# Kernel optimization log

Hardware: AMD Instinct MI355X
Metric: run time of the kernel (lower is better)

The kernel has to match this reference:

```python
import jax, jax.numpy as jnp
from jax import lax
import numpy as np

# GatedLinearAttention: S_t = alpha_t * S_{t-1} + k_t^T v_t ; o_t = q_t @ S_t
DIM = 1024
H = 8
DK = 128   # dim*expand_k(1.0)/H
DV = 256   # dim*expand_v(2.0)/H
GATE_NORM = 16.0

def setup_inputs() -> dict:
    key = jax.random.key(0)
    ks = jax.random.split(key, 8)
    B, S = 2, 4096
    def xavier(k, shape, gain=1.0):
        fan_in, fan_out = shape[0], shape[1]
        lim = gain * np.sqrt(6.0 / (fan_in + fan_out))
        return jax.random.uniform(k, shape, jnp.float32, -lim, lim)
    g = 2 ** (-2.5)
    # weights stored as [in, out] so y = x @ W (transpose of torch Linear storage)
    return {
        "x":   jax.random.normal(ks[0], (B, S, DIM), jnp.float32),
        "Wq":  xavier(ks[1], (DIM, H * DK), g),
        "Wk":  xavier(ks[2], (DIM, H * DK), g),
        "Wv":  xavier(ks[3], (DIM, H * DV), g),
        "Wo":  xavier(ks[4], (H * DV, DIM)),
        "Wg":  xavier(ks[5], (DIM, H)),
        "bg":  jnp.zeros((H,), jnp.float32),
        "Wog": xavier(ks[6], (DIM, H * DV)),
    }

def _gla(x, Wq, Wk, Wv, Wo, Wg, bg, Wog):
    B, S, D = x.shape
    q = (x @ Wq).reshape(B, S, H, DK)
    k = (x @ Wk).reshape(B, S, H, DK) * (DK ** -0.5)
    v = (x @ Wv).reshape(B, S, H, DV)
    alpha = jax.nn.sigmoid((x @ Wg + bg) / GATE_NORM)  # [B,S,H]

    def step(state, inp):
        qt, kt, vt, at = inp  # [B,H,dk], [B,H,dk], [B,H,dv], [B,H]
        state = at[..., None, None] * state + kt[..., None] * vt[:, :, None, :]
        out_t = jnp.einsum('bhk,bhkv->bhv', qt, state)
        return state, out_t

    state0 = jnp.zeros((B, H, DK, DV), x.dtype)
    xs = (jnp.moveaxis(q, 1, 0), jnp.moveaxis(k, 1, 0),
          jnp.moveaxis(v, 1, 0), jnp.moveaxis(alpha, 1, 0))
    _, outs = lax.scan(step, state0, xs)          # [S,B,H,dv]
    out = jnp.moveaxis(outs, 0, 1).reshape(B, S, H * DV)
    og = jax.nn.sigmoid(x @ Wog)
    return (out * og) @ Wo

def reference(x, Wq, Wk, Wv, Wo, Wg, bg, Wog):
    return _gla(x, Wq, Wk, Wv, Wo, Wg, bg, Wog)
```

## Files before the change

### kernel.cpp

```cpp
#include <hip/hip_runtime.h>
#include <cstdint>
#include <cstddef>

typedef unsigned short u16;
typedef unsigned int   u32;
typedef __attribute__((ext_vector_type(8))) short short8;
typedef __attribute__((ext_vector_type(4))) float f32x4;

__device__ __forceinline__ u16 f2bf(float f) {
    union { float f; u32 u; } v; v.f = f;
    u32 r = v.u + 0x7fffu + ((v.u >> 16) & 1u);
    return (u16)(r >> 16);
}
__device__ __forceinline__ float bf2f(u16 b) {
    union { u32 u; float f; } v; v.u = ((u32)b) << 16;
    return v.f;
}

__device__ __forceinline__ void gload16(const u16* g, u16* l) {
    __builtin_amdgcn_global_load_lds(
        (const __attribute__((address_space(1))) u32*)g,
        (__attribute__((address_space(3))) u32*)l,
        16, 0, 0);
}

#define SEQ   4096
#define BATCH 2
#define NH    8
#define DKH   128
#define DVH   256
#define DMODEL 1024
#define NPROJ 6144
#define CHUNK 64
#define NCHUNK (SEQ / CHUNK)

#define OFF_XB    0u
#define OFF_WCAT  16777216u
#define OFF_WOT   29360128u
#define OFF_PROJ  33554432u
#define OFF_L2A   134217728u
#define OFF_GC    134479872u
#define OFF_U     134483968u
#define OFF_Z     201592832u

__global__ __launch_bounds__(256) void cvt_x_kernel(const float* __restrict__ x,
                                                    u16* __restrict__ xb) {
    int i = (blockIdx.x * 256 + threadIdx.x) * 4;
    float4 v = *(const float4*)(x + i);
    u16 o[4] = { f2bf(v.x), f2bf(v.y), f2bf(v.z), f2bf(v.w) };
    *(uint2*)(xb + i) = *(const uint2*)o;
}

__global__ __launch_bounds__(256) void transpose_w(const float* __restrict__ W, int N, int K,
                                                   u16* __restrict__ outp, float scale) {
    __shared__ float t[32][33];
    int n0 = blockIdx.x * 32, k0 = blockIdx.y * 32;
    int tx = threadIdx.x, ty = threadIdx.y;
    #pragma unroll
    for (int j = 0; j < 4; ++j)
        t[ty + j * 8][tx] = W[(size_t)(k0 + ty + j * 8) * N + n0 + tx];
    __syncthreads();
    #pragma unroll
    for (int j = 0; j < 4; ++j)
        outp[(size_t)(n0 + ty + j * 8) * K + k0 + tx] = f2bf(t[tx][ty + j * 8] * scale);
}

__global__ __launch_bounds__(256) void alpha_kernel(const float* __restrict__ x,
                                                    const float* __restrict__ Wg,
                                                    const float* __restrict__ bg,
                                                    float* __restrict__ l2a) {
    __shared__ float xr[DMODEL];
    int row = blockIdx.x;
    for (int i = threadIdx.x; i < DMODEL; i += 256) xr[i] = x[(size_t)row * DMODEL + i];
    __syncthreads();
    int wave = threadIdx.x >> 6, lane = threadIdx.x & 63;
    #pragma unroll
    for (int hh = 0; hh < 2; ++hh) {
        int h = wave * 2 + hh;
        float p = 0.f;
        for (int i = lane; i < DMODEL; i += 64) p += xr[i] * Wg[i * NH + h];
        #pragma unroll
        for (int d = 32; d; d >>= 1) p += __shfl_down(p, d, 64);
        if (lane == 0) {
            float zz = (p + bg[h]) * (1.0f / 16.0f);
            float a = 1.0f / (1.0f + expf(-zz));
            l2a[row * NH + h] = log2f(a);
        }
    }
}

template <int EPI>
__global__ __launch_bounds__(512, 2) void gemm256(const u16* __restrict__ A, int lda,
                                                  const u16* __restrict__ B, int ldb,
                                                  void* __restrict__ Cout, int ldc,
                                                  int K, int nTN, int og_start) {
    __shared__ u16 lds[65536];
    const int tid = threadIdx.x;
    const int lane = tid & 63, wid = tid >> 6;
    const int wr = wid >> 2, wc = wid & 3;
    const int cpx = gridDim.x >> 3;
    const int wg = (blockIdx.x & 7) * cpx + (blockIdx.x >> 3);
    const int m0 = (wg / nTN) * 256, n0 = (wg % nTN) * 256;

    const int rsub = tid >> 2;
    const int ql = (tid & 3) ^ ((tid >> 4) & 3);
    const size_t ag0 = (size_t)(m0 + rsub) * lda + ql * 8;
    const size_t ag1 = (size_t)(m0 + 128 + rsub) * lda + ql * 8;
    const size_t bg0 = (size_t)(n0 + rsub) * ldb + ql * 8;
    const size_t bg1 = (size_t)(n0 + 128 + rsub) * ldb + ql * 8;
    const int sdw = wid * 512;

#define STG_A(t_, h_) gload16(A + ((h_) ? ag1 : ag0) + (size_t)(t_) * 32, \
                              lds + ((t_) & 3) * 8192 + (h_) * 4096 + sdw)
#define STG_B(t_, h_) gload16(B + ((h_) ? bg1 : bg0) + (size_t)(t_) * 32, \
                              lds + 32768 + ((t_) & 3) * 8192 + (h_) * 4096 + sdw)

    const int qr = ((lane >> 4) ^ ((lane >> 2) & 3)) * 8;
    const int arow = (wr * 128 + (lane & 15)) * 32 + qr;
    const int brow = 32768 + (wc * 64 + (lane & 15)) * 32 + qr;

    STG_A(0, 0); STG_A(0, 1); STG_B(0, 0); STG_B(0, 1);
    STG_A(1, 0); STG_A(1, 1); STG_B(1, 0); STG_B(1, 1);
    asm volatile("s_waitcnt vmcnt(4)\n\ts_barrier" ::: "memory");

    f32x4 acc[8][4] = {};
    const int NT = K >> 5;
    for (int t = 0; t < NT; ++t) {
        const u16* buf = lds + (t & 3) * 8192;
        const bool pre = (t + 2) < NT;
        if (pre) { STG_A(t + 2, 0); STG_A(t + 2, 1); }
        short8 bfr[4], afr[4];
        #pragma unroll
        for (int ct = 0; ct < 4; ++ct) bfr[ct] = *(const short8*)(buf + brow + ct * 512);
        #pragma unroll
        for (int rt = 0; rt < 4; ++rt) afr[rt] = *(const short8*)(buf + arow + rt * 512);
        __builtin_amdgcn_s_setprio(1);
        #pragma unroll
        for (int rt = 0; rt < 4; ++rt)
            #pragma unroll
            for (int ct = 0; ct < 4; ++ct)
                acc[rt][ct] = __builtin_amdgcn_mfma_f32_16x16x32_bf16(afr[rt], bfr[ct], acc[rt][ct], 0, 0, 0);
        __builtin_amdgcn_s_setprio(0);
        if (pre) { STG_B(t + 2, 0); STG_B(t + 2, 1); }
        #pragma unroll
        for (int rt = 0; rt < 4; ++rt) afr[rt] = *(const short8*)(buf + arow + (rt + 4) * 512);
        __builtin_amdgcn_s_setprio(1);
        #pragma unroll
        for (int rt = 0; rt < 4; ++rt)
            #pragma unroll
            for (int ct = 0; ct < 4; ++ct)
                acc[rt + 4][ct] = __builtin_amdgcn_mfma_f32_16x16x32_bf16(afr[rt], bfr[ct], acc[rt + 4][ct], 0, 0, 0);
        __builtin_amdgcn_s_setprio(0);
        if (t < NT - 2)       asm volatile("s_waitcnt vmcnt(4)\n\ts_barrier" ::: "memory");
        else if (t == NT - 2) asm volatile("s_waitcnt vmcnt(0)\n\ts_barrier" ::: "memory");
    }
#undef STG_A
#undef STG_B

    __syncthreads();
    if (EPI) {
        u16* Cw = lds + wid * 4608;
        #pragma unroll
        for (int pass = 0; pass < 2; ++pass) {
            #pragma unroll
            for (int rt = 0; rt < 4; ++rt)
                #pragma unroll
                for (int ct = 0; ct < 4; ++ct)
                    #pragma unroll
                    for (int j = 0; j < 4; ++j) {
                        int row = rt * 16 + (lane >> 4) * 4 + j;
                        int col = ct * 16 + (lane & 15);
                        float v = acc[pass * 4 + rt][ct][j];
                        if (n0 + wc * 64 + col >= og_start) v = 1.0f / (1.0f + expf(-v));
                        Cw[row * 72 + col] = f2bf(v);
                    }
            #pragma unroll
            for (int it = 0; it < 8; ++it) {
                int row = it * 8 + (lane >> 3);
                int c8 = (lane & 7) * 8;
                uint4 val = *reinterpret_cast<const uint4*>(&Cw[row * 72 + c8]);
                *reinterpret_cast<uint4*>((u16*)Cout +
                    (size_t)(m0 + wr * 128 + pass * 64 + row) * ldc + n0 + wc * 64 + c8) = val;
            }
        }
    } else {
        #pragma unroll
        for (int rt = 0; rt < 8; ++rt)
            #pragma unroll
            for (int ct = 0; ct < 4; ++ct)
                #pragma unroll
                for (int j = 0; j < 4; ++j) {
                    int m = m0 + wr * 128 + rt * 16 + (lane >> 4) * 4 + j;
                    int n = n0 + wc * 64 + ct * 16 + (lane & 15);
                    ((float*)Cout)[(size_t)m * ldc + n] = acc[rt][ct][j];
                }
    }
}

template <int EPI>
__global__ __launch_bounds__(256) void gemm_glds(const u16* __restrict__ A, int lda,
                                                 const u16* __restrict__ B, int ldb,
                                                 void* __restrict__ Cout, int ldc,
                                                 int K, int og_start) {
    __shared__ u16 smem[18432];
    u16* As = smem;
    u16* Bs = smem + 4096;
    const int tid = threadIdx.x;
    const int lane = tid & 63, wave = tid >> 6;
    const int m0 = blockIdx.y * 128, n0 = blockIdx.x * 128;
    const int m_off = (wave & 1) * 64, n_off = (wave >> 1) * 64;
    const int r = tid >> 2, kg = (tid & 3) * 8;
    f32x4 acc[4][4] = {};
    for (int k0 = 0; k0 < K; k0 += 32) {
        #pragma unroll
        for (int i = 0; i < 2; ++i) {
            int row = i * 64 + r;
            gload16(A + (size_t)(m0 + row) * lda + k0 + kg, As + (i * 256 + (tid & 192)) * 8);
            gload16(B + (size_t)(n0 + row) * ldb + k0 + kg, Bs + (i * 256 + (tid & 192)) * 8);
        }
        __syncthreads();
        short8 a[4], b[4];
        #pragma unroll
        for (int rt = 0; rt < 4; ++rt)
            a[rt] = *reinterpret_cast<const short8*>(&As[(m_off + rt * 16 + (lane & 15)) * 32 + (lane >> 4) * 8]);
        #pragma unroll
        for (int ct = 0; ct < 4; ++ct)
            b[ct] = *reinterpret_cast<const short8*>(&Bs[(n_off + ct * 16 + (lane & 15)) * 32 + (lane >> 4) * 8]);
        #pragma unroll
        for (int rt = 0; rt < 4; ++rt)
            #pragma unroll
            for (int ct = 0; ct < 4; ++ct)
                acc[rt][ct] = __builtin_amdgcn_mfma_f32_16x16x32_bf16(a[rt], b[ct], acc[rt][ct], 0, 0, 0);
        __syncthreads();
    }
    if (EPI) {
        u16* Cw = smem + wave * 4608;
        #pragma unroll
        for (int rt = 0; rt < 4; ++rt)
            #pragma unroll
            for (int ct = 0; ct < 4; ++ct)
                #pragma unroll
                for (int j = 0; j < 4; ++j) {
                    int row = rt * 16 + (lane >> 4) * 4 + j;
                    int col = ct * 16 + (lane & 15);
                    int n = n0 + n_off + col;
                    float v = acc[rt][ct][j];
                    if (n >= og_start) v = 1.0f / (1.0f + expf(-v));
                    Cw[row * 72 + col] = f2bf(v);
                }
        #pragma unroll
        for (int it = 0; it < 8; ++it) {
            int row = it * 8 + (lane >> 3);
            int c8 = (lane & 7) * 8;
            uint4 val = *reinterpret_cast<const uint4*>(&Cw[row * 72 + c8]);
            *reinterpret_cast<uint4*>((u16*)Cout + (size_t)(m0 + m_off + row) * ldc + n0 + n_off + c8) = val;
        }
    } else {
        #pragma unroll
        for (int rt = 0; rt < 4; ++rt)
            #pragma unroll
            for (int ct = 0; ct < 4; ++ct)
                #pragma unroll
                for (int j = 0; j < 4; ++j) {
                    int m = m0 + m_off + rt * 16 + (lane >> 4) * 4 + j;
                    int n = n0 + n_off + ct * 16 + (lane & 15);
                    ((float*)Cout)[(size_t)m * ldc + n] = acc[rt][ct][j];
                }
    }
}

__global__ __launch_bounds__(256) void r1_kernel(const u16* __restrict__ proj,
                                                 const float* __restrict__ l2a,
                                                 u16* __restrict__ U,
                                                 float* __restrict__ Gc) {
    __shared__ u16 kT[128 * 72];
    __shared__ u16 vT[256 * 72];
    __shared__ float Wsh[64];
    int bid = blockIdx.x;
    int c = bid & 63, bh = bid >> 6;
    int b = bh >> 3, h = bh & 7;
    int c0 = c * CHUNK;
    int tid = threadIdx.x, lane = tid & 63, wave = tid >> 6;
    size_t rowbase = (size_t)b * SEQ + c0;
    if (wave == 0) {
        float L = l2a[(rowbase + lane) * NH + h];
        #pragma unroll
        for (int d = 1; d < 64; d <<= 1) {
            float u = __shfl_up(L, d, 64);
            if (lane >= d) L += u;
        }
        float Lend = __shfl(L, 63, 64);
        Wsh[lane] = exp2f(Lend - L);
        if (lane == 0) Gc[bh * NCHUNK + c] = exp2f(Lend);
    }
    __syncthreads();
    #pragma unroll
    for (int j = 0; j < 4; ++j) {
        int cid = tid + j * 256;
        int s = cid >> 4, r = (cid & 15) * 8;
        uint4 v = *(const uint4*)(proj + (rowbase + s) * NPROJ + 1024 + h * DKH + r);
        u16 e[8]; *(uint4*)e = v;
        #pragma unroll
        for (int i = 0; i < 8; ++i) kT[(r + i) * 72 + s] = e[i];
    }
    #pragma unroll
    for (int j = 0; j < 8; ++j) {
        int cid = tid + j * 256;
        int s = cid >> 5, cc = (cid & 31) * 8;
        float w = Wsh[s];
        uint4 v = *(const uint4*)(proj + (rowbase + s) * NPROJ + 2048 + h * DVH + cc);
        u16 e[8]; *(uint4*)e = v;
        #pragma unroll
        for (int i = 0; i < 8; ++i) vT[(cc + i) * 72 + s] = f2bf(bf2f(e[i]) * w);
    }
    __syncthreads();
    short8 afr[4][2];
    #pragma unroll
    for (int rt = 0; rt < 4; ++rt)
        #pragma unroll
        for (int kk = 0; kk < 2; ++kk)
            afr[rt][kk] = *reinterpret_cast<const short8*>(
                &vT[(wave * 64 + rt * 16 + (lane & 15)) * 72 + kk * 32 + (lane >> 4) * 8]);
    size_t ubase = (size_t)(bh * NCHUNK + c) * (DVH * DKH);
    #pragma unroll
    for (int ct = 0; ct < 8; ++ct) {
        f32x4 acc[4] = {};
        #pragma unroll
        for (int kk = 0; kk < 2; ++kk) {
            short8 bfr = *reinterpret_cast<const short8*>(
                &kT[(ct * 16 + (lane & 15)) * 72 + kk * 32 + (lane >> 4) * 8]);
            #pragma unroll
            for (int rt = 0; rt < 4; ++rt)
                acc[rt] = __builtin_amdgcn_mfma_f32_16x16x32_bf16(afr[rt][kk], bfr, acc[rt], 0, 0, 0);
        }
        #pragma unroll
        for (int rt = 0; rt < 4; ++rt)
            #pragma unroll
            for (int j = 0; j < 4; ++j) {
                int ccr = wave * 64 + rt * 16 + (lane >> 4) * 4 + j;
                int rr = ct * 16 + (lane & 15);
                U[ubase + (size_t)ccr * DKH + rr] = f2bf(acc[rt][j]);
            }
    }
}

__global__ __launch_bounds__(256) void r2_kernel(u16* __restrict__ U, const float* __restrict__ Gc) {
    int bh = blockIdx.x >> 5;
    int e0 = ((blockIdx.x & 31) * 256 + threadIdx.x) * 4;
    const float* g = Gc + bh * NCHUNK;
    size_t base = (size_t)bh * NCHUNK * (DVH * DKH) + e0;
    float s0 = 0.f, s1 = 0.f, s2 = 0.f, s3 = 0.f;
    for (int c = 0; c < NCHUNK; ++c) {
        u16* p = U + base + (size_t)c * (DVH * DKH);
        uint2 u = *(const uint2*)p;
        u16 e[4]; *(uint2*)e = u;
        u16 o[4] = { f2bf(s0), f2bf(s1), f2bf(s2), f2bf(s3) };
        *(uint2*)p = *(const uint2*)o;
        float G = g[c];
        s0 = G * s0 + bf2f(e[0]);
        s1 = G * s1 + bf2f(e[1]);
        s2 = G * s2 + bf2f(e[2]);
        s3 = G * s3 + bf2f(e[3]);
    }
}

__global__ __launch_bounds__(256) void r3_kernel(const u16* __restrict__ proj,
                                                 const u16* __restrict__ Sp,
                                                 const float* __restrict__ l2a,
                                                 u16* __restrict__ z) {
    __shared__ u16 vT[256 * 72];
    __shared__ u16 P[64 * 72];
    __shared__ float Lsh[64];
    int bid = blockIdx.x;
    int c = bid & 63, bh = bid >> 6;
    int b = bh >> 3, h = bh & 7;
    int c0 = c * CHUNK;
    int tid = threadIdx.x, lane = tid & 63, wave = tid >> 6;
    size_t rowbase = (size_t)b * SEQ + c0;
    if (wave == 0) {
        float L = l2a[(rowbase + lane) * NH + h];
        #pragma unroll
        for (int d = 1; d < 64; d <<= 1) {
            float u = __shfl_up(L, d, 64);
            if (lane >= d) L += u;
        }
        Lsh[lane] = L;
    }
    #pragma unroll
    for (int j = 0; j < 8; ++j) {
        int cid = tid + j * 256;
        int s = cid >> 5, cc = (cid & 31) * 8;
        uint4 v = *(const uint4*)(proj + (rowbase + s) * NPROJ + 2048 + h * DVH + cc);
        u16 e[8]; *(uint4*)e = v;
        #pragma unroll
        for (int i = 0; i < 8; ++i) vT[(cc + i) * 72 + s] = e[i];
    }
    __syncthreads();
    {
        f32x4 pacc[4] = {};
        #pragma unroll
        for (int kk = 0; kk < 4; ++kk) {
            short8 a = *reinterpret_cast<const short8*>(
                proj + (rowbase + wave * 16 + (lane & 15)) * NPROJ + h * DKH + kk * 32 + (lane >> 4) * 8);
            #pragma unroll
            for (int st = 0; st < 4; ++st) {
                short8 bb = *reinterpret_cast<const short8*>(
                    proj + (rowbase + st * 16 + (lane & 15)) * NPROJ + 1024 + h * DKH + kk * 32 + (lane >> 4) * 8);
                pacc[st] = __builtin_amdgcn_mfma_f32_16x16x32_bf16(a, bb, pacc[st], 0, 0, 0);
            }
        }
        #pragma unroll
        for (int st = 0; st < 4; ++st)
            #pragma unroll
            for (int j = 0; j < 4; ++j) {
                int t = wave * 16 + (lane >> 4) * 4 + j;
                int s = st * 16 + (lane & 15);
                float val = pacc[st][j];
                val = (s <= t) ? val * exp2f(Lsh[t] - Lsh[s]) : 0.f;
                P[t * 72 + s] = f2bf(val);
            }
    }
    f32x4 acc[4][4] = {};
    size_t spbase = (size_t)(bh * NCHUNK + c) * (DVH * DKH);
    #pragma unroll
    for (int kk = 0; kk < 4; ++kk) {
        short8 a[4];
        #pragma unroll
        for (int rt = 0; rt < 4; ++rt)
            a[rt] = *reinterpret_cast<const short8*>(
                proj + (rowbase + rt * 16 + (lane & 15)) * NPROJ + h * DKH + kk * 32 + (lane >> 4) * 8);
        #pragma unroll
        for (int ct = 0; ct < 4; ++ct) {
            short8 bb = *reinterpret_cast<const short8*>(
                Sp + spbase + (size_t)(wave * 64 + ct * 16 + (lane & 15)) * DKH + kk * 32 + (lane >> 4) * 8);
            #pragma unroll
            for (int rt = 0; rt < 4; ++rt)
                acc[rt][ct] = __builtin_amdgcn_mfma_f32_16x16x32_bf16(a[rt], bb, acc[rt][ct], 0, 0, 0);
        }
    }
    #pragma unroll
    for (int rt = 0; rt < 4; ++rt)
        #pragma unroll
        for (int j = 0; j < 4; ++j) {
            float at = exp2f(Lsh[rt * 16 + (lane >> 4) * 4 + j]);
            #pragma unroll
            for (int ct = 0; ct < 4; ++ct) acc[rt][ct][j] *= at;
        }
    __syncthreads();
    #pragma unroll
    for (int kk = 0; kk < 2; ++kk) {
        short8 pa[4];
        #pragma unroll
        for (int rt = 0; rt < 4; ++rt)
            pa[rt] = *reinterpret_cast<const short8*>(&P[(rt * 16 + (lane & 15)) * 72 + kk * 32 + (lane >> 4) * 8]);
        #pragma unroll
        for (int ct = 0; ct < 4; ++ct) {
            short8 vb = *reinterpret_cast<const short8*>(
                &vT[(wave * 64 + ct * 16 + (lane & 15)) * 72 + kk * 32 + (lane >> 4) * 8]);
            #pragma unroll
            for (int rt = 0; rt < 4; ++rt)
                acc[rt][ct] = __builtin_amdgcn_mfma_f32_16x16x32_bf16(pa[rt], vb, acc[rt][ct], 0, 0, 0);
        }
    }
    #pragma unroll
    for (int rt = 0; rt < 4; ++rt)
        #pragma unroll
        for (int ct = 0; ct < 4; ++ct)
            #pragma unroll
            for (int j = 0; j < 4; ++j) {
                int t = rt * 16 + (lane >> 4) * 4 + j;
                int cc = wave * 64 + ct * 16 + (lane & 15);
                float og = bf2f(proj[(rowbase + t) * NPROJ + 4096 + h * DVH + cc]);
                float v = acc[rt][ct][j] * og;
                z[(rowbase + t) * (NH * DVH) + h * DVH + cc] = f2bf(v);
            }
}

extern "C" void kernel_launch(void* const* d_in, const int* in_sizes, int n_in,
                              void* d_out, int out_size, void* d_ws, size_t ws_size,
                              hipStream_t stream) {
    const float* x   = (const float*)d_in[0];
    const float* Wq  = (const float*)d_in[1];
    const float* Wk  = (const float*)d_in[2];
    const float* Wv  = (const float*)d_in[3];
    const float* Wo  = (const float*)d_in[4];
    const float* Wg  = (const float*)d_in[5];
    const float* bg  = (const float*)d_in[6];
    const float* Wog = (const float*)d_in[7];
    float* out = (float*)d_out;
    char* ws = (char*)d_ws;

    u16*   xb   = (u16*)(ws + OFF_XB);
    u16*   wcat = (u16*)(ws + OFF_WCAT);
    u16*   wot  = (u16*)(ws + OFF_WOT);
    u16*   proj = (u16*)(ws + OFF_PROJ);
    float* l2a  = (float*)(ws + OFF_L2A);
    float* gc   = (float*)(ws + OFF_GC);
    u16*   U    = (u16*)(ws + OFF_U);
    u16*   z    = (u16*)(ws + OFF_Z);

    cvt_x_kernel<<<8192, 256, 0, stream>>>(x, xb);
    dim3 tb(32, 8);
    transpose_w<<<dim3(32, 32), tb, 0, stream>>>(Wq,  1024, 1024, wcat,               1.0f);
    transpose_w<<<dim3(32, 32), tb, 0, stream>>>(Wk,  1024, 1024, wcat + 1024 * 1024, 0.08838834764831845f);
    transpose_w<<<dim3(64, 32), tb, 0, stream>>>(Wv,  2048, 1024, wcat + 2048 * 1024, 1.0f);
    transpose_w<<<dim3(64, 32), tb, 0, stream>>>(Wog, 2048, 1024, wcat + 4096 * 1024, 1.0f);
    transpose_w<<<dim3(32, 64), tb, 0, stream>>>(Wo,  1024, 2048, wot,                1.0f);
    alpha_kernel<<<8192, 256, 0, stream>>>(x, Wg, bg, l2a);
    gemm256<1><<<768, 512, 0, stream>>>(xb, 1024, wcat, 1024, proj, NPROJ, 1024, 24, 4096);
    r1_kernel<<<BATCH * NH * NCHUNK, 256, 0, stream>>>(proj, l2a, U, gc);
    r2_kernel<<<512, 256, 0, stream>>>(U, gc);
    r3_kernel<<<BATCH * NH * NCHUNK, 256, 0, stream>>>(proj, U, l2a, z);
    gemm_glds<0><<<dim3(8, 64), 256, 0, stream>>>(z, 2048, wot, 2048, out, 1024, 2048, 1 << 30);
}
```

Baseline: 586.5 us.

## Deepen GEMM LDS pipeline, double-buffer A fragments, and swizzle transposed LDS tiles

The GEMM now prefetches three K-tiles ahead instead of two and preloads the next tile's A fragments into registers while the current tile's MFMAs run, with the loop unrolled by two to ping-pong between register sets. It also changes the XOR swizzle used for global-to-LDS staging and reads, and widens the epilogue staging stride from 72 to 80. The chunk kernels write the transposed k and v tiles into LDS with an XOR-swizzled column offset so the scattered transposed writes and fragment reads conflict less on banks. The costs are higher register pressure from holding 16 A fragments per thread, and a 4-buffer ring with 3 tiles in flight that has tighter reuse, which makes correctness of the wait counts subtle.

```diff
diff --git a/kernel.cpp b/kernel.cpp
--- a/kernel.cpp
+++ b/kernel.cpp
@@ -103,7 +103,7 @@
     const int m0 = (wg / nTN) * 256, n0 = (wg % nTN) * 256;
 
     const int rsub = tid >> 2;
-    const int ql = (tid & 3) ^ ((tid >> 4) & 3);
+    const int ql = (tid & 3) ^ ((tid >> 3) & 3);
     const size_t ag0 = (size_t)(m0 + rsub) * lda + ql * 8;
     const size_t ag1 = (size_t)(m0 + 128 + rsub) * lda + ql * 8;
     const size_t bg0 = (size_t)(n0 + rsub) * ldb + ql * 8;
@@ -115,51 +115,62 @@
 #define STG_B(t_, h_) gload16(B + ((h_) ? bg1 : bg0) + (size_t)(t_) * 32, \
                               lds + 32768 + ((t_) & 3) * 8192 + (h_) * 4096 + sdw)
 
-    const int qr = ((lane >> 4) ^ ((lane >> 2) & 3)) * 8;
+    const int qr = ((lane >> 4) ^ ((lane >> 1) & 3)) * 8;
     const int arow = (wr * 128 + (lane & 15)) * 32 + qr;
     const int brow = 32768 + (wc * 64 + (lane & 15)) * 32 + qr;
 
+    const int NT = K >> 5;
     STG_A(0, 0); STG_A(0, 1); STG_B(0, 0); STG_B(0, 1);
     STG_A(1, 0); STG_A(1, 1); STG_B(1, 0); STG_B(1, 1);
+    STG_A(2, 0); STG_A(2, 1); STG_B(2, 0); STG_B(2, 1);
     asm volatile("s_waitcnt vmcnt(4)\n\ts_barrier" ::: "memory");
 
     f32x4 acc[8][4] = {};
-    const int NT = K >> 5;
-    for (int t = 0; t < NT; ++t) {
-        const u16* buf = lds + (t & 3) * 8192;
-        const bool pre = (t + 2) < NT;
-        if (pre) { STG_A(t + 2, 0); STG_A(t + 2, 1); }
-        short8 bfr[4], afr[4];
-        #pragma unroll
-        for (int ct = 0; ct < 4; ++ct) bfr[ct] = *(const short8*)(buf + brow + ct * 512);
-        #pragma unroll
-        for (int rt = 0; rt < 4; ++rt) afr[rt] = *(const short8*)(buf + arow + rt * 512);
-        __builtin_amdgcn_s_setprio(1);
-        #pragma unroll
-        for (int rt = 0; rt < 4; ++rt)
-            #pragma unroll
-            for (int ct = 0; ct < 4; ++ct)
-                acc[rt][ct] = __builtin_amdgcn_mfma_f32_16x16x32_bf16(afr[rt], bfr[ct], acc[rt][ct], 0, 0, 0);
-        __builtin_amdgcn_s_setprio(0);
-        if (pre) { STG_B(t + 2, 0); STG_B(t + 2, 1); }
-        #pragma unroll
-        for (int rt = 0; rt < 4; ++rt) afr[rt] = *(const short8*)(buf + arow + (rt + 4) * 512);
-        __builtin_amdgcn_s_setprio(1);
-        #pragma unroll
-        for (int rt = 0; rt < 4; ++rt)
-            #pragma unroll
-            for (int ct = 0; ct < 4; ++ct)
-                acc[rt + 4][ct] = __builtin_amdgcn_mfma_f32_16x16x32_bf16(afr[rt], bfr[ct], acc[rt + 4][ct], 0, 0, 0);
-        __builtin_amdgcn_s_setprio(0);
-        if (t < NT - 2)       asm volatile("s_waitcnt vmcnt(4)\n\ts_barrier" ::: "memory");
-        else if (t == NT - 2) asm volatile("s_waitcnt vmcnt(0)\n\ts_barrier" ::: "memory");
-    }
+    short8 aC[8], aN[8];
+    #pragma unroll
+    for (int rt = 0; rt < 8; ++rt) aC[rt] = *(const short8*)(lds + arow + rt * 512);
+
+#define TILE_BODY(T_, AC_, AN_) do {                                                   \
+    const u16* buf  = lds + ((T_) & 3) * 8192;                                         \
+    const u16* bufn = lds + (((T_) + 1) & 3) * 8192;                                   \
+    if ((T_) + 3 < NT) { STG_A((T_) + 3, 0); STG_A((T_) + 3, 1); }                     \
+    short8 bfr[4];                                                                     \
+    _Pragma("unroll")                                                                  \
+    for (int ct = 0; ct < 4; ++ct) bfr[ct] = *(const short8*)(buf + brow + ct * 512);  \
+    _Pragma("unroll")                                                                  \
+    for (int rt = 0; rt < 4; ++rt) AN_[rt] = *(const short8*)(bufn + arow + rt * 512); \
+    __builtin_amdgcn_s_setprio(1);                                                     \
+    _Pragma("unroll")                                                                  \
+    for (int rt = 0; rt < 4; ++rt)                                                     \
+        _Pragma("unroll")                                                              \
+        for (int ct = 0; ct < 4; ++ct)                                                 \
+            acc[rt][ct] = __builtin_amdgcn_mfma_f32_16x16x32_bf16(AC_[rt], bfr[ct], acc[rt][ct], 0, 0, 0); \
+    __builtin_amdgcn_s_setprio(0);                                                     \
+    if ((T_) + 3 < NT) { STG_B((T_) + 3, 0); STG_B((T_) + 3, 1); }                     \
+    _Pragma("unroll")                                                                  \
+    for (int rt = 0; rt < 4; ++rt) AN_[rt + 4] = *(const short8*)(bufn + arow + (rt + 4) * 512); \
+    __builtin_amdgcn_s_setprio(1);                                                     \
+    _Pragma("unroll")                                                                  \
+    for (int rt = 0; rt < 4; ++rt)                                                     \
+        _Pragma("unroll")                                                              \
+        for (int ct = 0; ct < 4; ++ct)                                                 \
+            acc[rt + 4][ct] = __builtin_amdgcn_mfma_f32_16x16x32_bf16(AC_[rt + 4], bfr[ct], acc[rt + 4][ct], 0, 0, 0); \
+    __builtin_amdgcn_s_setprio(0);                                                     \
+    if ((T_) + 3 < NT)      asm volatile("s_waitcnt vmcnt(4)\n\ts_barrier" ::: "memory"); \
+    else if ((T_) < NT - 1) asm volatile("s_waitcnt vmcnt(0)\n\ts_barrier" ::: "memory"); \
+} while (0)
+
+    for (int t = 0; t < NT; t += 2) {
+        TILE_BODY(t, aC, aN);
+        TILE_BODY(t + 1, aN, aC);
+    }
+#undef TILE_BODY
 #undef STG_A
 #undef STG_B
 
     __syncthreads();
     if (EPI) {
-        u16* Cw = lds + wid * 4608;
+        u16* Cw = lds + wid * 5120;
         #pragma unroll
         for (int pass = 0; pass < 2; ++pass) {
             #pragma unroll
@@ -172,13 +183,13 @@
                         int col = ct * 16 + (lane & 15);
                         float v = acc[pass * 4 + rt][ct][j];
                         if (n0 + wc * 64 + col >= og_start) v = 1.0f / (1.0f + expf(-v));
-                        Cw[row * 72 + col] = f2bf(v);
+                        Cw[row * 80 + col] = f2bf(v);
                     }
             #pragma unroll
             for (int it = 0; it < 8; ++it) {
                 int row = it * 8 + (lane >> 3);
                 int c8 = (lane & 7) * 8;
-                uint4 val = *reinterpret_cast<const uint4*>(&Cw[row * 72 + c8]);
+                uint4 val = *reinterpret_cast<const uint4*>(&Cw[row * 80 + c8]);
                 *reinterpret_cast<uint4*>((u16*)Cout +
                     (size_t)(m0 + wr * 128 + pass * 64 + row) * ldc + n0 + wc * 64 + c8) = val;
             }
@@ -298,37 +309,42 @@
     for (int j = 0; j < 4; ++j) {
         int cid = tid + j * 256;
         int s = cid >> 4, r = (cid & 15) * 8;
+        int ko = (s & 7) | ((((s >> 3) ^ cid) & 7) << 3);
         uint4 v = *(const uint4*)(proj + (rowbase + s) * NPROJ + 1024 + h * DKH + r);
         u16 e[8]; *(uint4*)e = v;
         #pragma unroll
-        for (int i = 0; i < 8; ++i) kT[(r + i) * 72 + s] = e[i];
+        for (int i = 0; i < 8; ++i) kT[(r + i) * 72 + ko] = e[i];
     }
     #pragma unroll
     for (int j = 0; j < 8; ++j) {
         int cid = tid + j * 256;
         int s = cid >> 5, cc = (cid & 31) * 8;
         float w = Wsh[s];
+        int vo = (s & 7) | ((((s >> 3) ^ cid) & 7) << 3);
         uint4 v = *(const uint4*)(proj + (rowbase + s) * NPROJ + 2048 + h * DVH + cc);
         u16 e[8]; *(uint4*)e = v;
         #pragma unroll
-        for (int i = 0; i < 8; ++i) vT[(cc + i) * 72 + s] = f2bf(bf2f(e[i]) * w);
+        for (int i = 0; i < 8; ++i) vT[(cc + i) * 72 + vo] = f2bf(bf2f(e[i]) * w);
     }
     __syncthreads();
     short8 afr[4][2];
     #pragma unroll
     for (int rt = 0; rt < 4; ++rt)
         #pragma unroll
-        for (int kk = 0; kk < 2; ++kk)
-            afr[rt][kk] = *reinterpret_cast<const short8*>(
-                &vT[(wave * 64 + rt * 16 + (lane & 15)) * 72 + kk * 32 + (lane >> 4) * 8]);
+        for (int kk = 0; kk < 2; ++kk) {
+            int cA = wave * 64 + rt * 16 + (lane & 15);
+            int op = ((kk * 4 + (lane >> 4)) ^ ((cA >> 3) & 7)) * 8;
+            afr[rt][kk] = *reinterpret_cast<const short8*>(&vT[cA * 72 + op]);
+        }
     size_t ubase = (size_t)(bh * NCHUNK + c) * (DVH * DKH);
     #pragma unroll
     for (int ct = 0; ct < 8; ++ct) {
         f32x4 acc[4] = {};
         #pragma unroll
         for (int kk = 0; kk < 2; ++kk) {
-            short8 bfr = *reinterpret_cast<const short8*>(
-                &kT[(ct * 16 + (lane & 15)) * 72 + kk * 32 + (lane >> 4) * 8]);
+            int rB = ct * 16 + (lane & 15);
+            int op = ((kk * 4 + (lane >> 4)) ^ ((rB >> 3) & 7)) * 8;
+            short8 bfr = *reinterpret_cast<const short8*>(&kT[rB * 72 + op]);
             #pragma unroll
             for (int rt = 0; rt < 4; ++rt)
                 acc[rt] = __builtin_amdgcn_mfma_f32_16x16x32_bf16(afr[rt][kk], bfr, acc[rt], 0, 0, 0);
@@ -390,10 +406,11 @@
     for (int j = 0; j < 8; ++j) {
         int cid = tid + j * 256;
         int s = cid >> 5, cc = (cid & 31) * 8;
+        int vo = (s & 7) | ((((s >> 3) ^ cid) & 7) << 3);
         uint4 v = *(const uint4*)(proj + (rowbase + s) * NPROJ + 2048 + h * DVH + cc);
         u16 e[8]; *(uint4*)e = v;
         #pragma unroll
-        for (int i = 0; i < 8; ++i) vT[(cc + i) * 72 + s] = e[i];
+        for (int i = 0; i < 8; ++i) vT[(cc + i) * 72 + vo] = e[i];
     }
     __syncthreads();
     {
@@ -455,8 +472,9 @@
             pa[rt] = *reinterpret_cast<const short8*>(&P[(rt * 16 + (lane & 15)) * 72 + kk * 32 + (lane >> 4) * 8]);
         #pragma unroll
         for (int ct = 0; ct < 4; ++ct) {
-            short8 vb = *reinterpret_cast<const short8*>(
-                &vT[(wave * 64 + ct * 16 + (lane & 15)) * 72 + kk * 32 + (lane >> 4) * 8]);
+            int cV = wave * 64 + ct * 16 + (lane & 15);
+            int op = ((kk * 4 + (lane >> 4)) ^ ((cV >> 3) & 7)) * 8;
+            short8 vb = *reinterpret_cast<const short8*>(&vT[cV * 72 + op]);
             #pragma unroll
             for (int rt = 0; rt < 4; ++rt)
                 acc[rt][ct] = __builtin_amdgcn_mfma_f32_16x16x32_bf16(pa[rt], vb, acc[rt][ct], 0, 0, 0);
```

Result: faster. 549.3 us (-6.3%).

## Restructure GEMM pipeline to 64-wide K double-buffering and swizzle transposed LDS tiles

Applied to the files above, without the earlier changes.

The main GEMM switches from a four-slot ring of 32-wide K tiles to two 64-wide stages. Each stage is split into two 32-wide halves with interleaved loads, explicit barriers and waitcnts, and the LDS swizzle pattern is changed to match. The epilogue staging stride is widened from 72 to 80. The chunk kernels now XOR-swizzle the column offsets of the transposed kT/vT tiles on write and read, to cut LDS bank conflicts. The extra barriers per iteration may reduce overlap, and the new swizzles must stay consistent between writers and readers.

```diff
diff --git a/kernel.cpp b/kernel.cpp
--- a/kernel.cpp
+++ b/kernel.cpp
@@ -103,63 +103,92 @@
     const int m0 = (wg / nTN) * 256, n0 = (wg % nTN) * 256;
 
     const int rsub = tid >> 2;
-    const int ql = (tid & 3) ^ ((tid >> 4) & 3);
-    const size_t ag0 = (size_t)(m0 + rsub) * lda + ql * 8;
-    const size_t ag1 = (size_t)(m0 + 128 + rsub) * lda + ql * 8;
-    const size_t bg0 = (size_t)(n0 + rsub) * ldb + ql * 8;
-    const size_t bg1 = (size_t)(n0 + 128 + rsub) * ldb + ql * 8;
+    const int qg = (tid & 3) ^ ((tid >> 3) & 3);
     const int sdw = wid * 512;
 
-#define STG_A(t_, h_) gload16(A + ((h_) ? ag1 : ag0) + (size_t)(t_) * 32, \
-                              lds + ((t_) & 3) * 8192 + (h_) * 4096 + sdw)
-#define STG_B(t_, h_) gload16(B + ((h_) ? bg1 : bg0) + (size_t)(t_) * 32, \
-                              lds + 32768 + ((t_) & 3) * 8192 + (h_) * 4096 + sdw)
-
-    const int qr = ((lane >> 4) ^ ((lane >> 2) & 3)) * 8;
+#define STG_A(t_, kh_, h_) gload16(A + (size_t)(m0 + (h_) * 128 + rsub) * lda + (t_) * 64 + (kh_) * 32 + qg * 8, \
+                                   lds + ((t_) & 1) * 16384 + (kh_) * 8192 + (h_) * 4096 + sdw)
+#define STG_B(t_, kh_, h_) gload16(B + (size_t)(n0 + (h_) * 128 + rsub) * ldb + (t_) * 64 + (kh_) * 32 + qg * 8, \
+                                   lds + 32768 + ((t_) & 1) * 16384 + (kh_) * 8192 + (h_) * 4096 + sdw)
+#define BAR() asm volatile("s_barrier" ::: "memory")
+
+    const int qr = ((lane >> 4) ^ ((lane >> 1) & 3)) * 8;
     const int arow = (wr * 128 + (lane & 15)) * 32 + qr;
     const int brow = 32768 + (wc * 64 + (lane & 15)) * 32 + qr;
 
-    STG_A(0, 0); STG_A(0, 1); STG_B(0, 0); STG_B(0, 1);
-    STG_A(1, 0); STG_A(1, 1); STG_B(1, 0); STG_B(1, 1);
-    asm volatile("s_waitcnt vmcnt(4)\n\ts_barrier" ::: "memory");
+    const int NT = K >> 6;
+    STG_A(0, 0, 0); STG_A(0, 0, 1); STG_B(0, 0, 0); STG_B(0, 0, 1);
+    STG_A(0, 1, 0); STG_A(0, 1, 1); STG_B(0, 1, 0); STG_B(0, 1, 1);
+    asm volatile("s_waitcnt vmcnt(4)" ::: "memory"); BAR();
 
     f32x4 acc[8][4] = {};
-    const int NT = K >> 5;
     for (int t = 0; t < NT; ++t) {
-        const u16* buf = lds + (t & 3) * 8192;
-        const bool pre = (t + 2) < NT;
-        if (pre) { STG_A(t + 2, 0); STG_A(t + 2, 1); }
-        short8 bfr[4], afr[4];
-        #pragma unroll
-        for (int ct = 0; ct < 4; ++ct) bfr[ct] = *(const short8*)(buf + brow + ct * 512);
-        #pragma unroll
-        for (int rt = 0; rt < 4; ++rt) afr[rt] = *(const short8*)(buf + arow + rt * 512);
+        const int d = (t & 1) * 16384;
+        const bool pre = (t + 1) < NT;
+        short8 a[4], b[4];
+        if (pre) { STG_A(t + 1, 0, 0); STG_A(t + 1, 0, 1); }
+        #pragma unroll
+        for (int ct = 0; ct < 4; ++ct) b[ct] = *(const short8*)(lds + d + brow + ct * 512);
+        #pragma unroll
+        for (int rt = 0; rt < 4; ++rt) a[rt] = *(const short8*)(lds + d + arow + rt * 512);
+        BAR();
         __builtin_amdgcn_s_setprio(1);
         #pragma unroll
         for (int rt = 0; rt < 4; ++rt)
             #pragma unroll
             for (int ct = 0; ct < 4; ++ct)
-                acc[rt][ct] = __builtin_amdgcn_mfma_f32_16x16x32_bf16(afr[rt], bfr[ct], acc[rt][ct], 0, 0, 0);
+                acc[rt][ct] = __builtin_amdgcn_mfma_f32_16x16x32_bf16(a[rt], b[ct], acc[rt][ct], 0, 0, 0);
         __builtin_amdgcn_s_setprio(0);
-        if (pre) { STG_B(t + 2, 0); STG_B(t + 2, 1); }
-        #pragma unroll
-        for (int rt = 0; rt < 4; ++rt) afr[rt] = *(const short8*)(buf + arow + (rt + 4) * 512);
+        BAR();
+        if (pre) { STG_B(t + 1, 0, 0); STG_B(t + 1, 0, 1); }
+        #pragma unroll
+        for (int rt = 0; rt < 4; ++rt) a[rt] = *(const short8*)(lds + d + arow + (rt + 4) * 512);
+        if (pre) asm volatile("s_waitcnt vmcnt(4)" ::: "memory");
+        else     asm volatile("s_waitcnt vmcnt(0)" ::: "memory");
+        BAR();
         __builtin_amdgcn_s_setprio(1);
         #pragma unroll
         for (int rt = 0; rt < 4; ++rt)
             #pragma unroll
             for (int ct = 0; ct < 4; ++ct)
-                acc[rt + 4][ct] = __builtin_amdgcn_mfma_f32_16x16x32_bf16(afr[rt], bfr[ct], acc[rt + 4][ct], 0, 0, 0);
+                acc[rt + 4][ct] = __builtin_amdgcn_mfma_f32_16x16x32_bf16(a[rt], b[ct], acc[rt + 4][ct], 0, 0, 0);
         __builtin_amdgcn_s_setprio(0);
-        if (t < NT - 2)       asm volatile("s_waitcnt vmcnt(4)\n\ts_barrier" ::: "memory");
-        else if (t == NT - 2) asm volatile("s_waitcnt vmcnt(0)\n\ts_barrier" ::: "memory");
+        BAR();
+        if (pre) { STG_A(t + 1, 1, 0); STG_A(t + 1, 1, 1); }
+        #pragma unroll
+        for (int ct = 0; ct < 4; ++ct) b[ct] = *(const short8*)(lds + d + 8192 + brow + ct * 512);
+        #pragma unroll
+        for (int rt = 0; rt < 4; ++rt) a[rt] = *(const short8*)(lds + d + 8192 + arow + rt * 512);
+        BAR();
+        __builtin_amdgcn_s_setprio(1);
+        #pragma unroll
+        for (int rt = 0; rt < 4; ++rt)
+            #pragma unroll
+            for (int ct = 0; ct < 4; ++ct)
+                acc[rt][ct] = __builtin_amdgcn_mfma_f32_16x16x32_bf16(a[rt], b[ct], acc[rt][ct], 0, 0, 0);
+        __builtin_amdgcn_s_setprio(0);
+        BAR();
+        if (pre) { STG_B(t + 1, 1, 0); STG_B(t + 1, 1, 1); }
+        #pragma unroll
+        for (int rt = 0; rt < 4; ++rt) a[rt] = *(const short8*)(lds + d + 8192 + arow + (rt + 4) * 512);
+        if (pre) asm volatile("s_waitcnt vmcnt(4)" ::: "memory");
+        BAR();
+        __builtin_amdgcn_s_setprio(1);
+        #pragma unroll
+        for (int rt = 0; rt < 4; ++rt)
+            #pragma unroll
+            for (int ct = 0; ct < 4; ++ct)
+                acc[rt + 4][ct] = __builtin_amdgcn_mfma_f32_16x16x32_bf16(a[rt], b[ct], acc[rt + 4][ct], 0, 0, 0);
+        __builtin_amdgcn_s_setprio(0);
+        BAR();
     }
 #undef STG_A
 #undef STG_B
+#undef BAR
 
     __syncthreads();
     if (EPI) {
-        u16* Cw = lds + wid * 4608;
+        u16* Cw = lds + wid * 5120;
         #pragma unroll
         for (int pass = 0; pass < 2; ++pass) {
             #pragma unroll
@@ -172,13 +201,13 @@
                         int col = ct * 16 + (lane & 15);
                         float v = acc[pass * 4 + rt][ct][j];
                         if (n0 + wc * 64 + col >= og_start) v = 1.0f / (1.0f + expf(-v));
-                        Cw[row * 72 + col] = f2bf(v);
+                        Cw[row * 80 + col] = f2bf(v);
                     }
             #pragma unroll
             for (int it = 0; it < 8; ++it) {
                 int row = it * 8 + (lane >> 3);
                 int c8 = (lane & 7) * 8;
-                uint4 val = *reinterpret_cast<const uint4*>(&Cw[row * 72 + c8]);
+                uint4 val = *reinterpret_cast<const uint4*>(&Cw[row * 80 + c8]);
                 *reinterpret_cast<uint4*>((u16*)Cout +
                     (size_t)(m0 + wr * 128 + pass * 64 + row) * ldc + n0 + wc * 64 + c8) = val;
             }
@@ -298,37 +327,42 @@
     for (int j = 0; j < 4; ++j) {
         int cid = tid + j * 256;
         int s = cid >> 4, r = (cid & 15) * 8;
+        int ko = (s & 7) | ((((s >> 3) ^ cid) & 7) << 3);
         uint4 v = *(const uint4*)(proj + (rowbase + s) * NPROJ + 1024 + h * DKH + r);
         u16 e[8]; *(uint4*)e = v;
         #pragma unroll
-        for (int i = 0; i < 8; ++i) kT[(r + i) * 72 + s] = e[i];
+        for (int i = 0; i < 8; ++i) kT[(r + i) * 72 + ko] = e[i];
     }
     #pragma unroll
     for (int j = 0; j < 8; ++j) {
         int cid = tid + j * 256;
         int s = cid >> 5, cc = (cid & 31) * 8;
         float w = Wsh[s];
+        int vo = (s & 7) | ((((s >> 3) ^ cid) & 7) << 3);
         uint4 v = *(const uint4*)(proj + (rowbase + s) * NPROJ + 2048 + h * DVH + cc);
         u16 e[8]; *(uint4*)e = v;
         #pragma unroll
-        for (int i = 0; i < 8; ++i) vT[(cc + i) * 72 + s] = f2bf(bf2f(e[i]) * w);
+        for (int i = 0; i < 8; ++i) vT[(cc + i) * 72 + vo] = f2bf(bf2f(e[i]) * w);
     }
     __syncthreads();
     short8 afr[4][2];
     #pragma unroll
     for (int rt = 0; rt < 4; ++rt)
         #pragma unroll
-        for (int kk = 0; kk < 2; ++kk)
-            afr[rt][kk] = *reinterpret_cast<const short8*>(
-                &vT[(wave * 64 + rt * 16 + (lane & 15)) * 72 + kk * 32 + (lane >> 4) * 8]);
+        for (int kk = 0; kk < 2; ++kk) {
+            int cA = wave * 64 + rt * 16 + (lane & 15);
+            int op = ((kk * 4 + (lane >> 4)) ^ ((cA >> 3) & 7)) * 8;
+            afr[rt][kk] = *reinterpret_cast<const short8*>(&vT[cA * 72 + op]);
+        }
     size_t ubase = (size_t)(bh * NCHUNK + c) * (DVH * DKH);
     #pragma unroll
     for (int ct = 0; ct < 8; ++ct) {
         f32x4 acc[4] = {};
         #pragma unroll
         for (int kk = 0; kk < 2; ++kk) {
-            short8 bfr = *reinterpret_cast<const short8*>(
-                &kT[(ct * 16 + (lane & 15)) * 72 + kk * 32 + (lane >> 4) * 8]);
+            int rB = ct * 16 + (lane & 15);
+            int op = ((kk * 4 + (lane >> 4)) ^ ((rB >> 3) & 7)) * 8;
+            short8 bfr = *reinterpret_cast<const short8*>(&kT[rB * 72 + op]);
             #pragma unroll
             for (int rt = 0; rt < 4; ++rt)
                 acc[rt] = __builtin_amdgcn_mfma_f32_16x16x32_bf16(afr[rt][kk], bfr, acc[rt], 0, 0, 0);
@@ -390,10 +424,11 @@
     for (int j = 0; j < 8; ++j) {
         int cid = tid + j * 256;
         int s = cid >> 5, cc = (cid & 31) * 8;
+        int vo = (s & 7) | ((((s >> 3) ^ cid) & 7) << 3);
         uint4 v = *(const uint4*)(proj + (rowbase + s) * NPROJ + 2048 + h * DVH + cc);
         u16 e[8]; *(uint4*)e = v;
         #pragma unroll
-        for (int i = 0; i < 8; ++i) vT[(cc + i) * 72 + s] = e[i];
+        for (int i = 0; i < 8; ++i) vT[(cc + i) * 72 + vo] = e[i];
     }
     __syncthreads();
     {
@@ -455,8 +490,9 @@
             pa[rt] = *reinterpret_cast<const short8*>(&P[(rt * 16 + (lane & 15)) * 72 + kk * 32 + (lane >> 4) * 8]);
         #pragma unroll
         for (int ct = 0; ct < 4; ++ct) {
-            short8 vb = *reinterpret_cast<const short8*>(
-                &vT[(wave * 64 + ct * 16 + (lane & 15)) * 72 + kk * 32 + (lane >> 4) * 8]);
+            int cV = wave * 64 + ct * 16 + (lane & 15);
+            int op = ((kk * 4 + (lane >> 4)) ^ ((cV >> 3) & 7)) * 8;
+            short8 vb = *reinterpret_cast<const short8*>(&vT[cV * 72 + op]);
             #pragma unroll
             for (int rt = 0; rt < 4; ++rt)
                 acc[rt][ct] = __builtin_amdgcn_mfma_f32_16x16x32_bf16(pa[rt], vb, acc[rt][ct], 0, 0, 0);
```

Result: faster. 561.1 us (-4.3%).
